# Kernel tuning notes

Hardware: AMD Instinct MI355X
Metric: run time of the kernel (lower is better)

Reference implementation:

```python
import jax, jax.numpy as jnp
import numpy as np
from functools import partial

N_NODES = 20000
N_EDGES = 640000
IN_C = 64
HID = 256
OUT_C = 64
HIST = 12
HORIZON = 6


def gcn_conv(x, w, b, src, dst, deg_inv, norm):
    # PyG GCNConv with self loops: out = D^-1/2 (A+I) D^-1/2 (x @ w) + b
    xw = x @ w                                   # [N, H]
    agg = jax.ops.segment_sum(xw[src] * norm[:, None], dst, num_segments=N_NODES)
    return agg + xw * deg_inv[:, None] + b


def gru_cell(x, h, wih, whh, bih, bhh):
    # torch.nn.GRUCell semantics; wih: [3H, in], whh: [3H, H]
    gi = x @ wih.T + bih
    gh = h @ whh.T + bhh
    ir, iz, inn = jnp.split(gi, 3, axis=-1)
    hr, hz, hn = jnp.split(gh, 3, axis=-1)
    r = jax.nn.sigmoid(ir + hr)
    z = jax.nn.sigmoid(iz + hz)
    n = jnp.tanh(inn + r * hn)
    return (1.0 - z) * n + z * h


def setup_inputs() -> dict:
    key = jax.random.key(0)
    ks = jax.random.split(key, 20)
    s = lambda fan: 1.0 / np.sqrt(fan)
    inp = {
        "x_seq": jax.random.normal(ks[0], (1, HIST, N_NODES, IN_C), dtype=jnp.float32),
        "src": jax.random.randint(ks[1], (N_EDGES,), 0, N_NODES),
        "dst": jax.random.randint(ks[2], (N_EDGES,), 0, N_NODES),
        "gcn1_w": jax.random.normal(ks[3], (IN_C, HID), jnp.float32) * s(IN_C),
        "gcn1_b": jnp.zeros((HID,), jnp.float32),
        "gcn2_w": jax.random.normal(ks[4], (HID, HID), jnp.float32) * s(HID),
        "gcn2_b": jnp.zeros((HID,), jnp.float32),
        "proj_w": jax.random.normal(ks[5], (HID, OUT_C), jnp.float32) * s(HID),
        "proj_b": jnp.zeros((OUT_C,), jnp.float32),
    }
    for i, name in enumerate(["gru1", "gru2", "gru3"]):
        k1, k2 = jax.random.split(ks[6 + i])
        inp[f"{name}_wih"] = jax.random.normal(k1, (3 * HID, HID), jnp.float32) * s(HID)
        inp[f"{name}_whh"] = jax.random.normal(k2, (3 * HID, HID), jnp.float32) * s(HID)
        inp[f"{name}_bih"] = jnp.zeros((3 * HID,), jnp.float32)
        inp[f"{name}_bhh"] = jnp.zeros((3 * HID,), jnp.float32)
    return inp


def reference(x_seq, src, dst, gcn1_w, gcn1_b, gcn2_w, gcn2_b, proj_w, proj_b,
              gru1_wih, gru1_whh, gru1_bih, gru1_bhh,
              gru2_wih, gru2_whh, gru2_bih, gru2_bhh,
              gru3_wih, gru3_whh, gru3_bih, gru3_bhh):
    # symmetric GCN normalization with self loops (static graph -> compute once)
    deg = jax.ops.segment_sum(jnp.ones((N_EDGES,), jnp.float32), dst, num_segments=N_NODES) + 1.0
    deg_is = deg ** -0.5
    norm = deg_is[src] * deg_is[dst]   # per-edge norm
    deg_inv = 1.0 / deg                # self-loop norm

    def cell(xt, h1, h2, h3):
        x = jax.nn.relu(gcn_conv(xt, gcn1_w, gcn1_b, src, dst, deg_inv, norm))
        x = jax.nn.relu(gcn_conv(x, gcn2_w, gcn2_b, src, dst, deg_inv, norm))
        h1 = gru_cell(x, h1, gru1_wih, gru1_whh, gru1_bih, gru1_bhh)
        h2 = gru_cell(h1, h2, gru2_wih, gru2_whh, gru2_bih, gru2_bhh)
        h3 = gru_cell(h2, h3, gru3_wih, gru3_whh, gru3_bih, gru3_bhh)
        return h1, h2, h3

    h0 = jnp.zeros((N_NODES, HID), jnp.float32)

    def enc_step(carry, xt):
        return cell(xt, *carry), None

    (h1, h2, h3), _ = jax.lax.scan(enc_step, (h0, h0, h0), x_seq[0])  # [T,N,C]

    def dec_step(carry, _):
        h1, h2, h3, xd = carry
        h1, h2, h3 = cell(xd, h1, h2, h3)
        y = h3 @ proj_w + proj_b       # [N, OUT_C]
        return (h1, h2, h3, y), y

    _, ys = jax.lax.scan(dec_step, (h1, h2, h3, x_seq[0, -1]), None, length=HORIZON)
    return ys[None]  # [1, HORIZON, N, OUT_C]
```

## Files before the change

kernel.cpp:

```cpp
#include <hip/hip_runtime.h>

#define N_NODESC 20000
#define N_EDGESC 640000

typedef _Float16 f16;
typedef __attribute__((ext_vector_type(4))) _Float16 f16x4;
typedef __attribute__((ext_vector_type(8))) _Float16 f16x8;
typedef __attribute__((ext_vector_type(4))) float f32x4;

__device__ __forceinline__ f32x4 mfma16(f16x8 a, f16x8 b, f32x4 c){
  return __builtin_amdgcn_mfma_f32_16x16x32_f16(a, b, c, 0, 0, 0);
}
__device__ __forceinline__ float sigm(float x){ return 1.f/(1.f+__expf(-x)); }
__device__ __forceinline__ float tanh_(float x){
  x = fminf(fmaxf(x, -15.f), 15.f);
  float e = __expf(-2.f*x);
  return (1.f - e)/(1.f + e);
}
__device__ __forceinline__ void stage16(const void* g, void* l){
  __builtin_amdgcn_global_load_lds((const __attribute__((address_space(1))) unsigned int*)g,
                                   (__attribute__((address_space(3))) unsigned int*)l, 16, 0, 0);
}
#define SB       __builtin_amdgcn_sched_barrier(0)
#define AS_VM(n) do{ asm volatile("s_waitcnt vmcnt(" #n ")" ::: "memory"); SB; }while(0)
#define BAR      do{ __builtin_amdgcn_s_barrier(); SB; }while(0)

__global__ __launch_bounds__(256) void k_hist(const int* __restrict__ dst, int* __restrict__ cnt){
  int e = blockIdx.x*256 + threadIdx.x;
  if(e < N_EDGESC) atomicAdd(&cnt[dst[e]], 1);
}

__global__ __launch_bounds__(256) void k_scanA(const int* __restrict__ cnt,
    int* __restrict__ row_ptr, int* __restrict__ btot){
  __shared__ int ws[4];
  int b = blockIdx.x, t = threadIdx.x;
  int i = b*256 + t;
  int v = (i < N_NODESC) ? cnt[i] : 0;
  int lane = t&63, wv = t>>6;
  int incl = v;
  #pragma unroll
  for(int off=1; off<64; off<<=1){ int u = __shfl_up(incl, off); if(lane>=off) incl += u; }
  if(lane==63) ws[wv] = incl;
  __syncthreads();
  int woff = 0;
  for(int k=0;k<wv;k++) woff += ws[k];
  if(i < N_NODESC) row_ptr[i] = woff + incl - v;
  if(t == 255) btot[b] = woff + incl;
}

__global__ __launch_bounds__(128) void k_scanB(const int* __restrict__ btot,
    int* __restrict__ boff, int* __restrict__ row_ptr){
  __shared__ int s[128];
  int t = threadIdx.x;
  int orig = (t < 79) ? btot[t] : 0;
  s[t] = orig;
  __syncthreads();
  #pragma unroll
  for(int off=1; off<128; off<<=1){
    int u = (t>=off) ? s[t-off] : 0;
    __syncthreads();
    s[t] += u;
    __syncthreads();
  }
  if(t < 79) boff[t] = s[t] - orig;
  if(t == 0) row_ptr[N_NODESC] = N_EDGESC;
}

__global__ __launch_bounds__(256) void k_scanC(const int* __restrict__ cnt,
    const int* __restrict__ boff, int* __restrict__ row_ptr,
    float* __restrict__ deg_inv, float* __restrict__ deg_is){
  int i = blockIdx.x*256 + threadIdx.x;
  if(i >= N_NODESC) return;
  row_ptr[i] += boff[blockIdx.x];
  float d = (float)(cnt[i] + 1);
  deg_inv[i] = 1.f/d;
  deg_is[i]  = rsqrtf(d);
}

__global__ __launch_bounds__(256) void k_fill(const int* __restrict__ src, const int* __restrict__ dst,
    const int* __restrict__ row_ptr, int* __restrict__ cursor, const float* __restrict__ deg_is,
    int2* __restrict__ ev){
  int e = blockIdx.x*256 + threadIdx.x;
  if(e >= N_EDGESC) return;
  int d = dst[e], s = src[e];
  int p = atomicAdd(&cursor[d], 1);
  int2 v;
  v.x = s;
  v.y = __float_as_int(deg_is[s]*deg_is[d]);
  ev[row_ptr[d] + p] = v;
}

__global__ __launch_bounds__(256) void k_cvt(const float* __restrict__ x, f16* __restrict__ o, int n4){
  int i = blockIdx.x*256 + threadIdx.x;
  if(i >= n4) return;
  f32x4 v = *(const f32x4*)(x + (size_t)i*4);
  *(f16x4*)(o + (size_t)i*4) = __builtin_convertvector(v, f16x4);
}

__global__ __launch_bounds__(256) void k_pack(const float* __restrict__ w, f16* __restrict__ dstp,
    int K, int NO, int trans){
  int t = blockIdx.x*256 + threadIdx.x;
  if(t >= K*NO) return;
  int i = t&7, g = (t>>3)&3, rest = t>>5;
  int c = rest % NO, kb = rest / NO;
  int k = kb*32 + g*8 + i;
  float v = trans ? w[(size_t)c*K + k] : w[(size_t)k*NO + c];
  dstp[t] = (f16)v;
}

__global__ __launch_bounds__(256) void k_agg64(const f16* __restrict__ x,
    const int* __restrict__ row_ptr, const int2* __restrict__ ev,
    const float* __restrict__ deg_inv, f16* __restrict__ O){
  int n = (blockIdx.x*256 + threadIdx.x)>>6;
  int c = threadIdx.x&63;
  if(n >= N_NODESC) return;
  float acc = deg_inv[n]*(float)x[(size_t)n*64 + c];
  int e0 = row_ptr[n], e1 = row_ptr[n+1];
  int e = e0;
  for(; e+4<=e1; e+=4){
    int2 a=ev[e], b=ev[e+1], cc=ev[e+2], d=ev[e+3];
    float v0=(float)x[(size_t)a.x*64+c],  v1=(float)x[(size_t)b.x*64+c];
    float v2=(float)x[(size_t)cc.x*64+c], v3=(float)x[(size_t)d.x*64+c];
    acc += __int_as_float(a.y)*v0 + __int_as_float(b.y)*v1
         + __int_as_float(cc.y)*v2 + __int_as_float(d.y)*v3;
  }
  for(; e<e1; e++){ int2 a=ev[e]; acc += __int_as_float(a.y)*(float)x[(size_t)a.x*64+c]; }
  O[(size_t)n*64+c] = (f16)acc;
}

__global__ __launch_bounds__(256) void k_agg256(const f16* __restrict__ x1,
    const int* __restrict__ row_ptr, const int2* __restrict__ ev,
    const float* __restrict__ deg_inv, f16* __restrict__ O){
  int n = (blockIdx.x*256 + threadIdx.x)>>6;
  int lane = threadIdx.x&63;
  if(n >= N_NODESC) return;
  const f16x4* xv = (const f16x4*)x1;
  f32x4 acc = __builtin_convertvector(xv[(size_t)n*64 + lane], f32x4) * deg_inv[n];
  int e0 = row_ptr[n], e1 = row_ptr[n+1];
  int e = e0;
  for(; e+4<=e1; e+=4){
    int2 a=ev[e], b=ev[e+1], cc=ev[e+2], d=ev[e+3];
    f32x4 v0=__builtin_convertvector(xv[(size_t)a.x*64+lane],  f32x4);
    f32x4 v1=__builtin_convertvector(xv[(size_t)b.x*64+lane],  f32x4);
    f32x4 v2=__builtin_convertvector(xv[(size_t)cc.x*64+lane], f32x4);
    f32x4 v3=__builtin_convertvector(xv[(size_t)d.x*64+lane],  f32x4);
    acc += v0*__int_as_float(a.y); acc += v1*__int_as_float(b.y);
    acc += v2*__int_as_float(cc.y); acc += v3*__int_as_float(d.y);
  }
  for(; e<e1; e++){ int2 a=ev[e];
    acc += __builtin_convertvector(xv[(size_t)a.x*64+lane], f32x4)*__int_as_float(a.y); }
  ((f16x4*)O)[(size_t)n*64+lane] = __builtin_convertvector(acc, f16x4);
}

__global__ __launch_bounds__(256) void k_gcn1(const f16* __restrict__ A,
    const f16* __restrict__ Bp, const float* __restrict__ bias, f16* __restrict__ C){
  __shared__ f16x8 ldsv[512];
  char* lds = (char*)ldsv;
  const int tid = threadIdx.x, lane = tid&63, w = tid>>6, l15 = lane&15, q = lane>>4;
  const int m0 = blockIdx.x*64;
  int rg = m0 + lane; if(rg > N_NODESC-1) rg = N_NODESC-1;
  #pragma unroll
  for(int i=0;i<2;i++){
    int region = i*4 + w;
    int kbb = region>>2, qq = region&3;
    stage16((const char*)A + (size_t)rg*128 + kbb*64 + qq*16, lds + region*1024 + lane*16);
  }
  AS_VM(0);
  BAR;
  f32x4 acc[4][4];
  #pragma unroll
  for(int rt=0;rt<4;rt++)
    #pragma unroll
    for(int ct=0;ct<4;ct++) acc[rt][ct] = (f32x4){0.f,0.f,0.f,0.f};
  #pragma unroll
  for(int kb=0;kb<2;kb++){
    f16x8 bf[4];
    #pragma unroll
    for(int ct=0;ct<4;ct++){
      int c = w*64 + ct*16 + l15;
      bf[ct] = *(const f16x8*)(Bp + ((unsigned)(kb*256 + c)*4 + q)*8);
    }
    #pragma unroll
    for(int rt=0;rt<4;rt++){
      f16x8 ah = *(const f16x8*)(lds + (kb*4+q)*1024 + (rt*16+l15)*16);
      #pragma unroll
      for(int ct=0;ct<4;ct++)
        acc[rt][ct] = mfma16(ah, bf[ct], acc[rt][ct]);
    }
  }
  #pragma unroll
  for(int rt=0;rt<4;rt++)
    #pragma unroll
    for(int ct=0;ct<4;ct++){
      int c = w*64 + ct*16 + l15;
      float bv = bias[c];
      #pragma unroll
      for(int j=0;j<4;j++){
        int r = m0 + rt*16 + q*4 + j;
        if(r < N_NODESC) C[(size_t)r*256 + c] = (f16)fmaxf(acc[rt][ct][j] + bv, 0.f);
      }
    }
}

__global__ __launch_bounds__(256,3) void k_gcn2(const f16* __restrict__ A,
    const f16* __restrict__ Bp, const float* __restrict__ bias, f16* __restrict__ C){
  __shared__ f16x8 ldsv[2048];
  char* lds = (char*)ldsv;
  const int tid = threadIdx.x, lane = tid&63, w = tid>>6, l15 = lane&15, q = lane>>4;
  const int m0 = blockIdx.x*64;
  int rg = m0 + lane; if(rg > N_NODESC-1) rg = N_NODESC-1;
  const size_t abyte = (size_t)rg*512;
  #pragma unroll
  for(int kb=0;kb<8;kb++)
    stage16((const char*)A + abyte + kb*64 + w*16, lds + kb*4096 + w*1024 + lane*16);
  AS_VM(0);
  BAR;
  f32x4 acc[4][4];
  #pragma unroll
  for(int rt=0;rt<4;rt++)
    #pragma unroll
    for(int ct=0;ct<4;ct++) acc[rt][ct] = (f32x4){0.f,0.f,0.f,0.f};
  f16x8 bf[2][4];
  #pragma unroll
  for(int ct=0;ct<4;ct++){
    int c = w*64 + ct*16 + l15;
    bf[0][ct] = *(const f16x8*)(Bp + ((unsigned)(0*256 + c)*4 + q)*8);
  }
  #pragma unroll
  for(int kb=0;kb<8;kb++){
    const int rB = kb&1;
    if(kb<7){
      #pragma unroll
      for(int ct=0;ct<4;ct++){
        int c = w*64 + ct*16 + l15;
        bf[rB^1][ct] = *(const f16x8*)(Bp + ((unsigned)((kb+1)*256 + c)*4 + q)*8);
      }
    }
    #pragma unroll
    for(int rt=0;rt<4;rt++){
      f16x8 ah = *(const f16x8*)(lds + kb*4096 + q*1024 + (rt*16+l15)*16);
      #pragma unroll
      for(int ct=0;ct<4;ct++)
        acc[rt][ct] = mfma16(ah, bf[rB][ct], acc[rt][ct]);
    }
  }
  #pragma unroll
  for(int rt=0;rt<4;rt++)
    #pragma unroll
    for(int ct=0;ct<4;ct++){
      int c = w*64 + ct*16 + l15;
      float bv = bias[c];
      #pragma unroll
      for(int j=0;j<4;j++){
        int r = m0 + rt*16 + q*4 + j;
        if(r < N_NODESC) C[(size_t)r*256 + c] = (f16)fmaxf(acc[rt][ct][j] + bv, 0.f);
      }
    }
}

__global__ __launch_bounds__(256,2) void k_gru(
    const f16* __restrict__ X, const f16* __restrict__ H, f16* __restrict__ Nh,
    const f16* __restrict__ Wi, const f16* __restrict__ Wh,
    const float* __restrict__ bih, const float* __restrict__ bhh){
  __shared__ f16x8 ldsv[4096];
  char* lds = (char*)ldsv;
  const int NB = 1252, QQ = NB>>3, RR = NB&7;
  int bid = blockIdx.x;
  int xcd = bid & 7, jj = bid >> 3;
  int nid = (xcd < RR) ? xcd*(QQ+1) + jj : RR*(QQ+1) + (xcd-RR)*QQ + jj;
  const int m0 = (nid>>2)*64;
  const int cb = nid&3;
  const int tid = threadIdx.x, lane = tid&63, w = tid>>6, l15 = lane&15, q = lane>>4;
  const int cc = cb*64 + w*16 + l15;
  int rg = m0 + lane; if(rg > N_NODESC-1) rg = N_NODESC-1;
  const size_t abyte = (size_t)rg*512;
  const f16* pl[2] = {X, H};
  #pragma unroll
  for(int p=0;p<2;p++)
    #pragma unroll
    for(int kb=0;kb<8;kb++)
      stage16((const char*)pl[p] + abyte + kb*64 + w*16,
              lds + p*32768 + kb*4096 + w*1024 + lane*16);
  AS_VM(0);
  BAR;
  f32x4 acc[6][4];
  #pragma unroll
  for(int m=0;m<6;m++)
    #pragma unroll
    for(int rt=0;rt<4;rt++) acc[m][rt] = (f32x4){0.f,0.f,0.f,0.f};
  const unsigned wbase = (unsigned)cc*32 + q*8;
  f16x8 breg[2][6];
  {
    breg[0][0] = *(const f16x8*)(Wi + wbase);
    breg[0][1] = *(const f16x8*)(Wi + wbase + 8192);
    breg[0][2] = *(const f16x8*)(Wi + wbase + 16384);
    breg[0][3] = *(const f16x8*)(Wh + wbase);
    breg[0][4] = *(const f16x8*)(Wh + wbase + 8192);
    breg[0][5] = *(const f16x8*)(Wh + wbase + 16384);
  }
  #pragma unroll
  for(int kb=0;kb<8;kb++){
    const int rB = kb&1;
    if(kb<7){
      unsigned wo = wbase + (unsigned)(kb+1)*24576u;
      breg[rB^1][0] = *(const f16x8*)(Wi + wo);
      breg[rB^1][1] = *(const f16x8*)(Wi + wo + 8192);
      breg[rB^1][2] = *(const f16x8*)(Wi + wo + 16384);
      breg[rB^1][3] = *(const f16x8*)(Wh + wo);
      breg[rB^1][4] = *(const f16x8*)(Wh + wo + 8192);
      breg[rB^1][5] = *(const f16x8*)(Wh + wo + 16384);
    }
    #pragma unroll
    for(int rt=0;rt<4;rt++){
      const int ro = kb*4096 + q*1024 + (rt*16+l15)*16;
      f16x8 ax = *(const f16x8*)(lds + ro);
      f16x8 ah = *(const f16x8*)(lds + 32768 + ro);
      acc[0][rt] = mfma16(ax, breg[rB][0], acc[0][rt]);
      acc[1][rt] = mfma16(ax, breg[rB][1], acc[1][rt]);
      acc[2][rt] = mfma16(ax, breg[rB][2], acc[2][rt]);
      acc[3][rt] = mfma16(ah, breg[rB][3], acc[3][rt]);
      acc[4][rt] = mfma16(ah, breg[rB][4], acc[4][rt]);
      acc[5][rt] = mfma16(ah, breg[rB][5], acc[5][rt]);
    }
  }
  float bir=bih[cc], biz=bih[cc+256], bin=bih[cc+512];
  float bhr=bhh[cc], bhz=bhh[cc+256], bhn=bhh[cc+512];
  #pragma unroll
  for(int rt=0;rt<4;rt++){
    #pragma unroll
    for(int j=0;j<4;j++){
      int r = m0 + rt*16 + q*4 + j;
      if(r < N_NODESC){
        float ir=acc[0][rt][j], iz=acc[1][rt][j], in_=acc[2][rt][j];
        float hr=acc[3][rt][j], hz=acc[4][rt][j], hn=acc[5][rt][j];
        float rgt = sigm(ir+bir + hr+bhr);
        float zg = sigm(iz+biz + hz+bhz);
        float ng = tanh_(in_+bin + rgt*(hn+bhn));
        float ho = (float)H[(size_t)r*256 + cc];
        float v = (1.f-zg)*ng + zg*ho;
        Nh[(size_t)r*256 + cc] = (f16)v;
      }
    }
  }
}

__global__ __launch_bounds__(256,4) void k_proj(const f16* __restrict__ A,
    const f16* __restrict__ Bp, const float* __restrict__ bias,
    float* __restrict__ C, f16* __restrict__ Cf16){
  __shared__ f16x8 ldsv[2048];
  char* lds = (char*)ldsv;
  const int tid = threadIdx.x, lane = tid&63, w = tid>>6, l15 = lane&15, q = lane>>4;
  const int m0 = blockIdx.x*64;
  const int cc = w*16 + l15;
  int rg = m0 + lane; if(rg > N_NODESC-1) rg = N_NODESC-1;
  const size_t abyte = (size_t)rg*512;
  #pragma unroll
  for(int kb=0;kb<8;kb++)
    stage16((const char*)A + abyte + kb*64 + w*16, lds + kb*4096 + w*1024 + lane*16);
  AS_VM(0);
  BAR;
  f32x4 acc[4];
  #pragma unroll
  for(int rt=0;rt<4;rt++) acc[rt] = (f32x4){0.f,0.f,0.f,0.f};
  f16x8 bf[2];
  bf[0] = *(const f16x8*)(Bp + ((unsigned)(0*64 + cc)*4 + q)*8);
  #pragma unroll
  for(int kb=0;kb<8;kb++){
    const int rB = kb&1;
    if(kb<7)
      bf[rB^1] = *(const f16x8*)(Bp + ((unsigned)((kb+1)*64 + cc)*4 + q)*8);
    #pragma unroll
    for(int rt=0;rt<4;rt++){
      f16x8 ah = *(const f16x8*)(lds + kb*4096 + q*1024 + (rt*16+l15)*16);
      acc[rt] = mfma16(ah, bf[rB], acc[rt]);
    }
  }
  #pragma unroll
  for(int rt=0;rt<4;rt++){
    float bv = bias[cc];
    #pragma unroll
    for(int j=0;j<4;j++){
      int r = m0 + rt*16 + q*4 + j;
      if(r < N_NODESC){
        float v = acc[rt][j] + bv;
        C[(size_t)r*64 + cc] = v;
        Cf16[(size_t)r*64 + cc] = (f16)v;
      }
    }
  }
}

extern "C" void kernel_launch(void* const* d_in, const int* in_sizes, int n_in,
                              void* d_out, int out_size, void* d_ws, size_t ws_size,
                              hipStream_t stream){
  const float* x_seq  = (const float*)d_in[0];
  const int*   srcp   = (const int*)  d_in[1];
  const int*   dstp   = (const int*)  d_in[2];
  const float* gcn1_w = (const float*)d_in[3];
  const float* gcn1_b = (const float*)d_in[4];
  const float* gcn2_w = (const float*)d_in[5];
  const float* gcn2_b = (const float*)d_in[6];
  const float* proj_w = (const float*)d_in[7];
  const float* proj_b = (const float*)d_in[8];
  const float* wih[3] = {(const float*)d_in[9],  (const float*)d_in[13], (const float*)d_in[17]};
  const float* whh[3] = {(const float*)d_in[10], (const float*)d_in[14], (const float*)d_in[18]};
  const float* bih[3] = {(const float*)d_in[11], (const float*)d_in[15], (const float*)d_in[19]};
  const float* bhh[3] = {(const float*)d_in[12], (const float*)d_in[16], (const float*)d_in[20]};
  float* out = (float*)d_out;

  const size_t NP = (size_t)N_NODESC*256;
  char* p = (char*)d_ws;
  auto alloc = [&](size_t bytes)->char*{ char* r = p; p += (bytes + 255) & ~(size_t)255; return r; };
  int*   deg_cnt = (int*)  alloc((size_t)2*N_NODESC*4);
  int*   cursor  = deg_cnt + N_NODESC;
  int*   row_ptr = (int*)  alloc((size_t)(N_NODESC+1)*4);
  float* deg_inv = (float*)alloc((size_t)N_NODESC*4);
  float* deg_is  = (float*)alloc((size_t)N_NODESC*4);
  int*   btot    = (int*)  alloc((size_t)128*4);
  int*   boff    = (int*)  alloc((size_t)128*4);
  int2*  ev      = (int2*) alloc((size_t)N_EDGESC*8);
  f16* xf16 = (f16*)alloc((size_t)12*N_NODESC*64*2);
  f16* xdec = (f16*)alloc((size_t)N_NODESC*64*2);
  f16* z64  = (f16*)alloc((size_t)N_NODESC*64*2);
  f16* x1   = (f16*)alloc(NP*2);
  f16* xa   = (f16*)alloc(NP*2);
  f16* hbuf = (f16*)alloc((size_t)2*3*NP*2);
  f16* pk_gcn1 = (f16*)alloc((size_t)64*256*2);
  f16* pk_gcn2 = (f16*)alloc((size_t)256*256*2);
  f16* pk_proj = (f16*)alloc((size_t)256*64*2);
  f16* pk_wi[3]; f16* pk_wh[3];
  for(int i=0;i<3;i++){ pk_wi[i]=(f16*)alloc((size_t)256*768*2); pk_wh[i]=(f16*)alloc((size_t)256*768*2); }

  hipMemsetAsync(deg_cnt, 0, (size_t)2*N_NODESC*4, stream);
  hipMemsetAsync(hbuf,    0, (size_t)3*NP*2, stream);

  k_hist <<<2500,256,0,stream>>>(dstp, deg_cnt);
  k_scanA<<<79,  256,0,stream>>>(deg_cnt, row_ptr, btot);
  k_scanB<<<1,   128,0,stream>>>(btot, boff, row_ptr);
  k_scanC<<<79,  256,0,stream>>>(deg_cnt, boff, row_ptr, deg_inv, deg_is);
  k_fill <<<2500,256,0,stream>>>(srcp, dstp, row_ptr, cursor, deg_is, ev);
  k_cvt  <<<15000,256,0,stream>>>(x_seq, xf16, 12*N_NODESC*64/4);

  k_pack<<<64, 256,0,stream>>>(gcn1_w, pk_gcn1, 64, 256, 0);
  k_pack<<<256,256,0,stream>>>(gcn2_w, pk_gcn2, 256,256, 0);
  k_pack<<<64, 256,0,stream>>>(proj_w, pk_proj, 256, 64, 0);
  for(int i=0;i<3;i++){
    k_pack<<<768,256,0,stream>>>(wih[i], pk_wi[i], 256, 768, 1);
    k_pack<<<768,256,0,stream>>>(whh[i], pk_wh[i], 256, 768, 1);
  }

  auto Hs = [&](int slot, int g)->f16*{ return hbuf + ((size_t)(slot*3+g))*NP; };

  for(int s=0; s<18; s++){
    const f16* xt;
    if(s < 12)       xt = xf16 + (size_t)s*N_NODESC*64;
    else if(s == 12) xt = xf16 + (size_t)11*N_NODESC*64;
    else             xt = xdec;
    int cur = s&1, nxt = cur^1;

    k_agg64 <<<5000,256,0,stream>>>(xt, row_ptr, ev, deg_inv, z64);
    k_gcn1  <<<313, 256,0,stream>>>(z64, pk_gcn1, gcn1_b, x1);
    k_agg256<<<5000,256,0,stream>>>(x1, row_ptr, ev, deg_inv, xa);
    k_gcn2  <<<313, 256,0,stream>>>(xa, pk_gcn2, gcn2_b, xa);

    k_gru<<<1252,256,0,stream>>>(xa,        Hs(cur,0), Hs(nxt,0), pk_wi[0], pk_wh[0], bih[0], bhh[0]);
    k_gru<<<1252,256,0,stream>>>(Hs(nxt,0), Hs(cur,1), Hs(nxt,1), pk_wi[1], pk_wh[1], bih[1], bhh[1]);
    k_gru<<<1252,256,0,stream>>>(Hs(nxt,1), Hs(cur,2), Hs(nxt,2), pk_wi[2], pk_wh[2], bih[2], bhh[2]);

    if(s >= 12)
      k_proj<<<313,256,0,stream>>>(Hs(nxt,2), pk_proj, proj_b, out + (size_t)(s-12)*N_NODESC*64, xdec);
  }
}
```

Before: 3.787 ms.

## Fuse GCN2, three GRU cells and projection into one per-tile mega kernel

Replaces the separate gcn2, three GRU and projection launches with one kernel. Each 64-row tile keeps its activations and hidden states in LDS, chains all phases with block barriers, and loops over the four column groups inside the block. This removes the intermediate global round trips and several launches per step. In exchange, the large LDS footprint limits the kernel to one 4-wave block per CU over only 313 blocks. That lowers occupancy and latency hiding for the weight loads and leaves a tail on the last wave of blocks.

```diff
diff --git a/kernel.cpp b/kernel.cpp
--- a/kernel.cpp
+++ b/kernel.cpp
@@ -202,182 +202,138 @@
     }
 }
 
-__global__ __launch_bounds__(256,3) void k_gcn2(const f16* __restrict__ A,
-    const f16* __restrict__ Bp, const float* __restrict__ bias, f16* __restrict__ C){
-  __shared__ f16x8 ldsv[2048];
-  char* lds = (char*)ldsv;
-  const int tid = threadIdx.x, lane = tid&63, w = tid>>6, l15 = lane&15, q = lane>>4;
-  const int m0 = blockIdx.x*64;
-  int rg = m0 + lane; if(rg > N_NODESC-1) rg = N_NODESC-1;
-  const size_t abyte = (size_t)rg*512;
-  #pragma unroll
-  for(int kb=0;kb<8;kb++)
-    stage16((const char*)A + abyte + kb*64 + w*16, lds + kb*4096 + w*1024 + lane*16);
-  AS_VM(0);
-  BAR;
-  f32x4 acc[4][4];
-  #pragma unroll
-  for(int rt=0;rt<4;rt++)
-    #pragma unroll
-    for(int ct=0;ct<4;ct++) acc[rt][ct] = (f32x4){0.f,0.f,0.f,0.f};
-  f16x8 bf[2][4];
-  #pragma unroll
-  for(int ct=0;ct<4;ct++){
-    int c = w*64 + ct*16 + l15;
-    bf[0][ct] = *(const f16x8*)(Bp + ((unsigned)(0*256 + c)*4 + q)*8);
-  }
+
+__device__ __forceinline__ void stage_slot(const char* src, char* dst, int w, int lane){
+  #pragma unroll
+  for(int i=0;i<8;i++)
+    stage16(src + (i*4+w)*16, dst + (i*4+w)*1024 + lane*16);
+}
+
+__device__ __forceinline__ void gcn2_phase(char* lds, int sa, int so,
+    const f16* __restrict__ Bp, const float* __restrict__ bias,
+    int w, int l15, int q){
+  for(int cg=0; cg<4; ++cg){
+    const int cc = cg*64 + w*16 + l15;
+    f16x8 bf[2];
+    bf[0] = *(const f16x8*)(Bp + ((unsigned)cc*4 + q)*8);
+    f32x4 acc[4];
+    #pragma unroll
+    for(int rt=0;rt<4;rt++) acc[rt] = (f32x4){0.f,0.f,0.f,0.f};
+    #pragma unroll
+    for(int kb=0;kb<8;kb++){
+      const int rB = kb&1;
+      if(kb<7) bf[rB^1] = *(const f16x8*)(Bp + ((unsigned)((kb+1)*256 + cc)*4 + q)*8);
+      #pragma unroll
+      for(int rt=0;rt<4;rt++){
+        const int ro = (kb*4+q)*1024 + (rt*16+l15)*16;
+        f16x8 a = *(const f16x8*)(lds + sa + ro);
+        acc[rt] = mfma16(a, bf[rB], acc[rt]);
+      }
+    }
+    float bv = bias[cc];
+    const int ob = (cc>>3)*1024 + (cc&7)*2;
+    #pragma unroll
+    for(int rt=0;rt<4;rt++)
+      #pragma unroll
+      for(int j=0;j<4;j++){
+        int r = rt*16 + q*4 + j;
+        *(f16*)(lds + so + ob + r*16) = (f16)fmaxf(acc[rt][j] + bv, 0.f);
+      }
+  }
+}
+
+__device__ __forceinline__ void gru_phase(char* lds, int sa, int sh, int so,
+    const f16* __restrict__ Wi, const f16* __restrict__ Wh,
+    const float* __restrict__ bih, const float* __restrict__ bhh,
+    f16* __restrict__ Hnew, int m0, int w, int l15, int q){
+  for(int cg=0; cg<4; ++cg){
+    const int cc = cg*64 + w*16 + l15;
+    const unsigned wb = (unsigned)cc*32 + q*8;
+    f16x8 bi[2][3], bh[2][3];
+    bi[0][0] = *(const f16x8*)(Wi + wb);
+    bi[0][1] = *(const f16x8*)(Wi + wb + 8192);
+    bi[0][2] = *(const f16x8*)(Wi + wb + 16384);
+    bh[0][0] = *(const f16x8*)(Wh + wb);
+    bh[0][1] = *(const f16x8*)(Wh + wb + 8192);
+    bh[0][2] = *(const f16x8*)(Wh + wb + 16384);
+    f32x4 acc[6][4];
+    #pragma unroll
+    for(int m=0;m<6;m++)
+      #pragma unroll
+      for(int rt=0;rt<4;rt++) acc[m][rt] = (f32x4){0.f,0.f,0.f,0.f};
+    #pragma unroll
+    for(int kb=0;kb<8;kb++){
+      const int rB = kb&1;
+      if(kb<7){
+        unsigned wo = wb + (unsigned)(kb+1)*24576u;
+        bi[rB^1][0] = *(const f16x8*)(Wi + wo);
+        bi[rB^1][1] = *(const f16x8*)(Wi + wo + 8192);
+        bi[rB^1][2] = *(const f16x8*)(Wi + wo + 16384);
+        bh[rB^1][0] = *(const f16x8*)(Wh + wo);
+        bh[rB^1][1] = *(const f16x8*)(Wh + wo + 8192);
+        bh[rB^1][2] = *(const f16x8*)(Wh + wo + 16384);
+      }
+      #pragma unroll
+      for(int rt=0;rt<4;rt++){
+        const int ro = (kb*4+q)*1024 + (rt*16+l15)*16;
+        f16x8 ax = *(const f16x8*)(lds + sa + ro);
+        f16x8 ah = *(const f16x8*)(lds + sh + ro);
+        acc[0][rt] = mfma16(ax, bi[rB][0], acc[0][rt]);
+        acc[1][rt] = mfma16(ax, bi[rB][1], acc[1][rt]);
+        acc[2][rt] = mfma16(ax, bi[rB][2], acc[2][rt]);
+        acc[3][rt] = mfma16(ah, bh[rB][0], acc[3][rt]);
+        acc[4][rt] = mfma16(ah, bh[rB][1], acc[4][rt]);
+        acc[5][rt] = mfma16(ah, bh[rB][2], acc[5][rt]);
+      }
+    }
+    float bir=bih[cc], biz=bih[cc+256], bin=bih[cc+512];
+    float bhr=bhh[cc], bhz=bhh[cc+256], bhn=bhh[cc+512];
+    const int ob = (cc>>3)*1024 + (cc&7)*2;
+    #pragma unroll
+    for(int rt=0;rt<4;rt++){
+      #pragma unroll
+      for(int j=0;j<4;j++){
+        int r = rt*16 + q*4 + j;
+        float ir=acc[0][rt][j], iz=acc[1][rt][j], in_=acc[2][rt][j];
+        float hr=acc[3][rt][j], hz=acc[4][rt][j], hn=acc[5][rt][j];
+        float rg = sigm(ir+bir + hr+bhr);
+        float zg = sigm(iz+biz + hz+bhz);
+        float ng = tanh_(in_+bin + rg*(hn+bhn));
+        float ho = (float)*(const f16*)(lds + sh + ob + r*16);
+        float v = (1.f-zg)*ng + zg*ho;
+        f16 hv = (f16)v;
+        *(f16*)(lds + so + ob + r*16) = hv;
+        int grow = m0 + r;
+        if(grow < N_NODESC) Hnew[(size_t)grow*256 + cc] = hv;
+      }
+    }
+  }
+}
+
+__device__ __forceinline__ void proj_phase(char* lds, int sa,
+    const f16* __restrict__ Bp, const float* __restrict__ bias,
+    float* __restrict__ C, f16* __restrict__ Cf16,
+    int m0, int w, int l15, int q){
+  const int cc = w*16 + l15;
+  f16x8 bf[2];
+  bf[0] = *(const f16x8*)(Bp + ((unsigned)cc*4 + q)*8);
+  f32x4 acc[4];
+  #pragma unroll
+  for(int rt=0;rt<4;rt++) acc[rt] = (f32x4){0.f,0.f,0.f,0.f};
   #pragma unroll
   for(int kb=0;kb<8;kb++){
     const int rB = kb&1;
-    if(kb<7){
-      #pragma unroll
-      for(int ct=0;ct<4;ct++){
-        int c = w*64 + ct*16 + l15;
-        bf[rB^1][ct] = *(const f16x8*)(Bp + ((unsigned)((kb+1)*256 + c)*4 + q)*8);
-      }
-    }
+    if(kb<7) bf[rB^1] = *(const f16x8*)(Bp + ((unsigned)((kb+1)*64 + cc)*4 + q)*8);
     #pragma unroll
     for(int rt=0;rt<4;rt++){
-      f16x8 ah = *(const f16x8*)(lds + kb*4096 + q*1024 + (rt*16+l15)*16);
-      #pragma unroll
-      for(int ct=0;ct<4;ct++)
-        acc[rt][ct] = mfma16(ah, bf[rB][ct], acc[rt][ct]);
-    }
-  }
-  #pragma unroll
-  for(int rt=0;rt<4;rt++)
-    #pragma unroll
-    for(int ct=0;ct<4;ct++){
-      int c = w*64 + ct*16 + l15;
-      float bv = bias[c];
-      #pragma unroll
-      for(int j=0;j<4;j++){
-        int r = m0 + rt*16 + q*4 + j;
-        if(r < N_NODESC) C[(size_t)r*256 + c] = (f16)fmaxf(acc[rt][ct][j] + bv, 0.f);
-      }
-    }
-}
-
-__global__ __launch_bounds__(256,2) void k_gru(
-    const f16* __restrict__ X, const f16* __restrict__ H, f16* __restrict__ Nh,
-    const f16* __restrict__ Wi, const f16* __restrict__ Wh,
-    const float* __restrict__ bih, const float* __restrict__ bhh){
-  __shared__ f16x8 ldsv[4096];
-  char* lds = (char*)ldsv;
-  const int NB = 1252, QQ = NB>>3, RR = NB&7;
-  int bid = blockIdx.x;
-  int xcd = bid & 7, jj = bid >> 3;
-  int nid = (xcd < RR) ? xcd*(QQ+1) + jj : RR*(QQ+1) + (xcd-RR)*QQ + jj;
-  const int m0 = (nid>>2)*64;
-  const int cb = nid&3;
-  const int tid = threadIdx.x, lane = tid&63, w = tid>>6, l15 = lane&15, q = lane>>4;
-  const int cc = cb*64 + w*16 + l15;
-  int rg = m0 + lane; if(rg > N_NODESC-1) rg = N_NODESC-1;
-  const size_t abyte = (size_t)rg*512;
-  const f16* pl[2] = {X, H};
-  #pragma unroll
-  for(int p=0;p<2;p++)
-    #pragma unroll
-    for(int kb=0;kb<8;kb++)
-      stage16((const char*)pl[p] + abyte + kb*64 + w*16,
-              lds + p*32768 + kb*4096 + w*1024 + lane*16);
-  AS_VM(0);
-  BAR;
-  f32x4 acc[6][4];
-  #pragma unroll
-  for(int m=0;m<6;m++)
-    #pragma unroll
-    for(int rt=0;rt<4;rt++) acc[m][rt] = (f32x4){0.f,0.f,0.f,0.f};
-  const unsigned wbase = (unsigned)cc*32 + q*8;
-  f16x8 breg[2][6];
-  {
-    breg[0][0] = *(const f16x8*)(Wi + wbase);
-    breg[0][1] = *(const f16x8*)(Wi + wbase + 8192);
-    breg[0][2] = *(const f16x8*)(Wi + wbase + 16384);
-    breg[0][3] = *(const f16x8*)(Wh + wbase);
-    breg[0][4] = *(const f16x8*)(Wh + wbase + 8192);
-    breg[0][5] = *(const f16x8*)(Wh + wbase + 16384);
-  }
-  #pragma unroll
-  for(int kb=0;kb<8;kb++){
-    const int rB = kb&1;
-    if(kb<7){
-      unsigned wo = wbase + (unsigned)(kb+1)*24576u;
-      breg[rB^1][0] = *(const f16x8*)(Wi + wo);
-      breg[rB^1][1] = *(const f16x8*)(Wi + wo + 8192);
-      breg[rB^1][2] = *(const f16x8*)(Wi + wo + 16384);
-      breg[rB^1][3] = *(const f16x8*)(Wh + wo);
-      breg[rB^1][4] = *(const f16x8*)(Wh + wo + 8192);
-      breg[rB^1][5] = *(const f16x8*)(Wh + wo + 16384);
-    }
-    #pragma unroll
-    for(int rt=0;rt<4;rt++){
-      const int ro = kb*4096 + q*1024 + (rt*16+l15)*16;
-      f16x8 ax = *(const f16x8*)(lds + ro);
-      f16x8 ah = *(const f16x8*)(lds + 32768 + ro);
-      acc[0][rt] = mfma16(ax, breg[rB][0], acc[0][rt]);
-      acc[1][rt] = mfma16(ax, breg[rB][1], acc[1][rt]);
-      acc[2][rt] = mfma16(ax, breg[rB][2], acc[2][rt]);
-      acc[3][rt] = mfma16(ah, breg[rB][3], acc[3][rt]);
-      acc[4][rt] = mfma16(ah, breg[rB][4], acc[4][rt]);
-      acc[5][rt] = mfma16(ah, breg[rB][5], acc[5][rt]);
-    }
-  }
-  float bir=bih[cc], biz=bih[cc+256], bin=bih[cc+512];
-  float bhr=bhh[cc], bhz=bhh[cc+256], bhn=bhh[cc+512];
+      const int ro = (kb*4+q)*1024 + (rt*16+l15)*16;
+      f16x8 a = *(const f16x8*)(lds + sa + ro);
+      acc[rt] = mfma16(a, bf[rB], acc[rt]);
+    }
+  }
+  float bv = bias[cc];
   #pragma unroll
   for(int rt=0;rt<4;rt++){
-    #pragma unroll
-    for(int j=0;j<4;j++){
-      int r = m0 + rt*16 + q*4 + j;
-      if(r < N_NODESC){
-        float ir=acc[0][rt][j], iz=acc[1][rt][j], in_=acc[2][rt][j];
-        float hr=acc[3][rt][j], hz=acc[4][rt][j], hn=acc[5][rt][j];
-        float rgt = sigm(ir+bir + hr+bhr);
-        float zg = sigm(iz+biz + hz+bhz);
-        float ng = tanh_(in_+bin + rgt*(hn+bhn));
-        float ho = (float)H[(size_t)r*256 + cc];
-        float v = (1.f-zg)*ng + zg*ho;
-        Nh[(size_t)r*256 + cc] = (f16)v;
-      }
-    }
-  }
-}
-
-__global__ __launch_bounds__(256,4) void k_proj(const f16* __restrict__ A,
-    const f16* __restrict__ Bp, const float* __restrict__ bias,
-    float* __restrict__ C, f16* __restrict__ Cf16){
-  __shared__ f16x8 ldsv[2048];
-  char* lds = (char*)ldsv;
-  const int tid = threadIdx.x, lane = tid&63, w = tid>>6, l15 = lane&15, q = lane>>4;
-  const int m0 = blockIdx.x*64;
-  const int cc = w*16 + l15;
-  int rg = m0 + lane; if(rg > N_NODESC-1) rg = N_NODESC-1;
-  const size_t abyte = (size_t)rg*512;
-  #pragma unroll
-  for(int kb=0;kb<8;kb++)
-    stage16((const char*)A + abyte + kb*64 + w*16, lds + kb*4096 + w*1024 + lane*16);
-  AS_VM(0);
-  BAR;
-  f32x4 acc[4];
-  #pragma unroll
-  for(int rt=0;rt<4;rt++) acc[rt] = (f32x4){0.f,0.f,0.f,0.f};
-  f16x8 bf[2];
-  bf[0] = *(const f16x8*)(Bp + ((unsigned)(0*64 + cc)*4 + q)*8);
-  #pragma unroll
-  for(int kb=0;kb<8;kb++){
-    const int rB = kb&1;
-    if(kb<7)
-      bf[rB^1] = *(const f16x8*)(Bp + ((unsigned)((kb+1)*64 + cc)*4 + q)*8);
-    #pragma unroll
-    for(int rt=0;rt<4;rt++){
-      f16x8 ah = *(const f16x8*)(lds + kb*4096 + q*1024 + (rt*16+l15)*16);
-      acc[rt] = mfma16(ah, bf[rB], acc[rt]);
-    }
-  }
-  #pragma unroll
-  for(int rt=0;rt<4;rt++){
-    float bv = bias[cc];
     #pragma unroll
     for(int j=0;j<4;j++){
       int r = m0 + rt*16 + q*4 + j;
@@ -387,6 +343,49 @@
         Cf16[(size_t)r*64 + cc] = (f16)v;
       }
     }
+  }
+}
+
+__global__ __launch_bounds__(256,1) void k_mega(
+    const f16* __restrict__ za,
+    const f16* __restrict__ H1o, const f16* __restrict__ H2o, const f16* __restrict__ H3o,
+    f16* __restrict__ H1n, f16* __restrict__ H2n, f16* __restrict__ H3n,
+    const f16* __restrict__ W2p, const float* __restrict__ b2,
+    const f16* __restrict__ Wi1, const f16* __restrict__ Wh1,
+    const float* __restrict__ bi1, const float* __restrict__ bh1,
+    const f16* __restrict__ Wi2, const f16* __restrict__ Wh2,
+    const float* __restrict__ bi2, const float* __restrict__ bh2,
+    const f16* __restrict__ Wi3, const f16* __restrict__ Wh3,
+    const float* __restrict__ bi3, const float* __restrict__ bh3,
+    const f16* __restrict__ Pp, const float* __restrict__ pb,
+    float* __restrict__ Out, f16* __restrict__ Xdec, int do_proj){
+  __shared__ f16x8 ldsv[8192];
+  char* lds = (char*)ldsv;
+  const int NB = 313, QQ = NB>>3, RR = NB&7;
+  int bid = blockIdx.x;
+  int xcd = bid & 7, jj = bid >> 3;
+  int nid = (xcd < RR) ? xcd*(QQ+1) + jj : RR*(QQ+1) + (xcd-RR)*QQ + jj;
+  const int m0 = nid*64;
+  const int tid = threadIdx.x, lane = tid&63, w = tid>>6, l15 = lane&15, q = lane>>4;
+  int rg = m0 + lane; if(rg > N_NODESC-1) rg = N_NODESC-1;
+  const size_t rb = (size_t)rg*512;
+  const int S0 = 0, S1 = 32768, S2 = 65536, S3 = 98304;
+
+  stage_slot((const char*)za + rb, lds + S0, w, lane);
+  __syncthreads();
+  stage_slot((const char*)H1o + rb, lds + S1, w, lane);
+  stage_slot((const char*)H2o + rb, lds + S3, w, lane);
+  gcn2_phase(lds, S0, S2, W2p, b2, w, l15, q);
+  __syncthreads();
+  gru_phase(lds, S2, S1, S0, Wi1, Wh1, bi1, bh1, H1n, m0, w, l15, q);
+  __syncthreads();
+  stage_slot((const char*)H3o + rb, lds + S2, w, lane);
+  gru_phase(lds, S0, S3, S1, Wi2, Wh2, bi2, bh2, H2n, m0, w, l15, q);
+  __syncthreads();
+  gru_phase(lds, S1, S2, S3, Wi3, Wh3, bi3, bh3, H3n, m0, w, l15, q);
+  if(do_proj){
+    __syncthreads();
+    proj_phase(lds, S3, Pp, pb, Out, Xdec, m0, w, l15, q);
   }
 }
 
@@ -461,13 +460,16 @@
     k_agg64 <<<5000,256,0,stream>>>(xt, row_ptr, ev, deg_inv, z64);
     k_gcn1  <<<313, 256,0,stream>>>(z64, pk_gcn1, gcn1_b, x1);
     k_agg256<<<5000,256,0,stream>>>(x1, row_ptr, ev, deg_inv, xa);
-    k_gcn2  <<<313, 256,0,stream>>>(xa, pk_gcn2, gcn2_b, xa);
-
-    k_gru<<<1252,256,0,stream>>>(xa,        Hs(cur,0), Hs(nxt,0), pk_wi[0], pk_wh[0], bih[0], bhh[0]);
-    k_gru<<<1252,256,0,stream>>>(Hs(nxt,0), Hs(cur,1), Hs(nxt,1), pk_wi[1], pk_wh[1], bih[1], bhh[1]);
-    k_gru<<<1252,256,0,stream>>>(Hs(nxt,1), Hs(cur,2), Hs(nxt,2), pk_wi[2], pk_wh[2], bih[2], bhh[2]);
-
-    if(s >= 12)
-      k_proj<<<313,256,0,stream>>>(Hs(nxt,2), pk_proj, proj_b, out + (size_t)(s-12)*N_NODESC*64, xdec);
-  }
-}
+
+    k_mega<<<313,256,0,stream>>>(xa,
+        Hs(cur,0), Hs(cur,1), Hs(cur,2),
+        Hs(nxt,0), Hs(nxt,1), Hs(nxt,2),
+        pk_gcn2, gcn2_b,
+        pk_wi[0], pk_wh[0], bih[0], bhh[0],
+        pk_wi[1], pk_wh[1], bih[1], bhh[1],
+        pk_wi[2], pk_wh[2], bih[2], bhh[2],
+        pk_proj, proj_b,
+        (s >= 12) ? (out + (size_t)(s-12)*N_NODESC*64) : out,
+        xdec, (s >= 12) ? 1 : 0);
+  }
+}
```

Measured after the change: 5.918 ms. +56.3%, slower.
